# Kernel tuning notes

Hardware: AMD Instinct MI355X
Metric: run time of the kernel (lower is better)

The kernel has to match this reference:

```python
import jax, jax.numpy as jnp
import numpy as np
from jax import lax

L = 12        # transformer layers
H = 768       # d_model
NH = 12       # heads
HD = H // NH  # head dim
F = 2048      # ffn dim (torch TransformerEncoderLayer default)
V = 128       # vocab_size (level logits)
NLV = 128     # n_levels (rows of routed weight W)
B, S = 8, 512
EPS = 1e-5


def _layer_norm(x, g, b):
    mu = jnp.mean(x, axis=-1, keepdims=True)
    var = jnp.mean(jnp.square(x - mu), axis=-1, keepdims=True)
    return g * (x - mu) / jnp.sqrt(var + EPS) + b


def _encoder(x, layer_params):
    # torch nn.TransformerEncoderLayer, post-LN, ReLU, eval mode (no dropout)
    def block(h, p):
        Wqkv, bqkv, Wo, bo, g1, bb1, W1, b1f, W2, b2f, g2, bb2 = p
        qkv = h @ Wqkv.T + bqkv                      # [B,S,3H]
        q, k, v = jnp.split(qkv, 3, axis=-1)
        sh = (h.shape[0], h.shape[1], NH, HD)
        q, k, v = q.reshape(sh), k.reshape(sh), v.reshape(sh)
        scores = jnp.einsum('bqhd,bkhd->bhqk', q, k) / jnp.sqrt(jnp.asarray(HD, h.dtype))
        attn = jax.nn.softmax(scores, axis=-1)
        o = jnp.einsum('bhqk,bkhd->bqhd', attn, v).reshape(h.shape)
        o = o @ Wo.T + bo
        h = _layer_norm(h + o, g1, bb1)
        f = jnp.maximum(h @ W1.T + b1f, 0.0) @ W2.T + b2f
        h = _layer_norm(h + f, g2, bb2)
        return h, None
    x, _ = lax.scan(block, x, layer_params)
    return x


def setup_inputs() -> dict:
    key = jax.random.key(0)
    ks = jax.random.split(key, 20)
    s = 0.02
    rn = lambda k, shp: jax.random.normal(k, shp, jnp.float32) * s
    inp = {
        'level_ids': jax.random.randint(ks[0], (B, S), 0, V, jnp.int32),
        'sublevel_ids': jax.random.randint(ks[1], (B, S), 0, V, jnp.int32),
        'bin_emb': rn(ks[2], (V, H)),
        'sub_emb': rn(ks[3], (V, H)),
        'Wqkv': rn(ks[4], (L, 3 * H, H)),
        'bqkv': jnp.zeros((L, 3 * H), jnp.float32),
        'Wo': rn(ks[5], (L, H, H)),
        'bo': jnp.zeros((L, H), jnp.float32),
        'ln1_g': jnp.ones((L, H), jnp.float32),
        'ln1_b': jnp.zeros((L, H), jnp.float32),
        'W1': rn(ks[6], (L, F, H)),
        'b1': jnp.zeros((L, F), jnp.float32),
        'W2': rn(ks[7], (L, H, F)),
        'b2': jnp.zeros((L, H), jnp.float32),
        'ln2_g': jnp.ones((L, H), jnp.float32),
        'ln2_b': jnp.zeros((L, H), jnp.float32),
        'W_lm': rn(ks[8], (V, H)),
        'b_lm': jnp.zeros((V,), jnp.float32),
        'W': rn(ks[9], (NLV, H, V)),       # routed per-level weights
        'bias': jnp.zeros((NLV, V), jnp.float32),
    }
    return inp


def reference(level_ids, sublevel_ids, bin_emb, sub_emb, Wqkv, bqkv, Wo, bo,
              ln1_g, ln1_b, W1, b1, W2, b2, ln2_g, ln2_b, W_lm, b_lm, W, bias):
    # embedding: sum of two id tables (tabular bin/subbin embedding)
    x = bin_emb[level_ids] + sub_emb[sublevel_ids]            # [B,S,H]
    layer_params = (Wqkv, bqkv, Wo, bo, ln1_g, ln1_b, W1, b1, W2, b2, ln2_g, ln2_b)
    x = _encoder(x, layer_params)                              # [B,S,H]
    out = x @ W_lm.T + b_lm                                    # [B,S,V]
    ix = jnp.argmax(out, axis=-1)                              # [B,S] routing index
    # per-token weight gather + batched vec-mat: the irregular hot path
    Wg = W[ix]                                                 # [B,S,H,V]
    sublevel_out = jnp.einsum('bsh,bshv->bsv', x, Wg) + bias[ix]
    return (out, sublevel_out)
```

## Files before the change

### kernel.cpp

```cpp
#include <hip/hip_runtime.h>
#include <cstdint>
#include <cstddef>

#define TOK 4096
#define HD_ 64
#define NH_ 12
#define H_ 768
#define F_ 2048
#define V_ 128
#define L_ 12
#define SEQ 512
#define BQKV (3*H_)
#define BATCH 8

typedef _Float16 f16;
typedef _Float16 f16x8 __attribute__((ext_vector_type(8)));
typedef _Float16 f16x4 __attribute__((ext_vector_type(4)));
typedef float    f32x4 __attribute__((ext_vector_type(4)));

#define GLDS16(g, l) __builtin_amdgcn_global_load_lds( \
    (const __attribute__((address_space(1))) uint32_t*)(g), \
    (__attribute__((address_space(3))) uint32_t*)(l), 16, 0, 0)

__device__ __forceinline__ float wave_sum(float v) {
#pragma unroll
  for (int m = 32; m >= 1; m >>= 1) v += __shfl_xor(v, m);
  return v;
}

__device__ __forceinline__ void split16(float v, f16& h, f16& lo) {
  h = (f16)v;
  lo = (f16)((v - (float)h) * 2048.0f);
}

__device__ __forceinline__ int swz(int r, int c) {
  int byte = (r << 7) + (c << 1);
  byte ^= (r & 7) << 4;
  return byte >> 1;
}

__global__ __launch_bounds__(256)
void k_convert(const float* __restrict__ src, f16* __restrict__ h, f16* __restrict__ l,
               int n4, float scale) {
  int i = blockIdx.x * 256 + threadIdx.x;
  int stride = gridDim.x * 256;
  for (; i < n4; i += stride) {
    float4 v = ((const float4*)src)[i];
    v.x *= scale; v.y *= scale; v.z *= scale; v.w *= scale;
    f16x4 vh, vl;
    f16 a, b;
    split16(v.x, a, b); vh[0] = a; vl[0] = b;
    split16(v.y, a, b); vh[1] = a; vl[1] = b;
    split16(v.z, a, b); vh[2] = a; vl[2] = b;
    split16(v.w, a, b); vh[3] = a; vl[3] = b;
    ((f16x4*)h)[i] = vh;
    ((f16x4*)l)[i] = vl;
  }
}

__global__ __launch_bounds__(256)
void k_embed2(const int* __restrict__ lid, const int* __restrict__ sid,
              const float* __restrict__ be, const float* __restrict__ se,
              float* __restrict__ x, f16* __restrict__ xh, f16* __restrict__ xl) {
  int t = blockIdx.x;
  int li = lid[t], si = sid[t];
  const float* bp = be + (size_t)li * H_;
  const float* sp = se + (size_t)si * H_;
  size_t base = (size_t)t * H_;
#pragma unroll
  for (int j = 0; j < 3; ++j) {
    int hh = threadIdx.x + 256 * j;
    float v = bp[hh] + sp[hh];
    x[base + hh] = v;
    f16 a, b; split16(v, a, b);
    xh[base + hh] = a; xl[base + hh] = b;
  }
}

template<int BM, int BN, int MODE>
__global__ __launch_bounds__(256)
void k_gemm3(const f16* __restrict__ Ah, const f16* __restrict__ Al,
             const f16* __restrict__ Bh, const f16* __restrict__ Bl,
             const float* __restrict__ bias, float* __restrict__ C,
             f16* __restrict__ Ch, f16* __restrict__ Cl,
             int N, int K) {
  constexpr int MI = BM / 32, NJ = BN / 32;
  constexpr int IA = BM / 64, IB = BN / 64;
  constexpr int ABYT = BM * 64, BBYT = BN * 64;
  constexpr int BUFB = 2 * ABYT + 2 * BBYT;
  __shared__ __align__(16) char sm[2 * BUFB];
  const int tid = threadIdx.x;
  const int lane = tid & 63, wid = tid >> 6;
  const int wr = wid >> 1, wc = wid & 1;
  const int bm = blockIdx.x * BM, bn = blockIdx.y * BN;
  const size_t rs = (size_t)K * 2;

  const int srow = tid >> 2, schk = tid & 3;
  const char* ga[2][IA];
  const char* gb[2][IB];
#pragma unroll
  for (int u = 0; u < IA; ++u) {
    int row = u * 64 + srow;
    int c = schk ^ ((row >> 1) & 3);
    ga[0][u] = (const char*)Ah + (size_t)(bm + row) * rs + c * 16;
    ga[1][u] = (const char*)Al + (size_t)(bm + row) * rs + c * 16;
  }
#pragma unroll
  for (int u = 0; u < IB; ++u) {
    int row = u * 64 + srow;
    int c = schk ^ ((row >> 1) & 3);
    gb[0][u] = (const char*)Bh + (size_t)(bn + row) * rs + c * 16;
    gb[1][u] = (const char*)Bl + (size_t)(bn + row) * rs + c * 16;
  }

  const int rr = lane & 15, cgrp = lane >> 4;
  int aoff[MI][2], boff[NJ][2];
#pragma unroll
  for (int i = 0; i < MI; ++i) {
    int row = wr * (BM / 2) + i * 16 + rr;
    int sw = (cgrp ^ ((row >> 1) & 3)) * 16;
    aoff[i][0] = row * 64 + sw;
    aoff[i][1] = ABYT + row * 64 + sw;
  }
#pragma unroll
  for (int j = 0; j < NJ; ++j) {
    int row = wc * (BN / 2) + j * 16 + rr;
    int sw = (cgrp ^ ((row >> 1) & 3)) * 16;
    boff[j][0] = 2 * ABYT + row * 64 + sw;
    boff[j][1] = 2 * ABYT + BBYT + row * 64 + sw;
  }

  f32x4 aH[MI][NJ], aM[MI][NJ];
#pragma unroll
  for (int i = 0; i < MI; ++i)
#pragma unroll
    for (int j = 0; j < NJ; ++j)
#pragma unroll
      for (int q = 0; q < 4; ++q) { aH[i][j][q] = 0.0f; aM[i][j][q] = 0.0f; }

  auto STG = [&](int b) __attribute__((always_inline)) {
    char* base = sm + b * BUFB + wid * 1024;
#pragma unroll
    for (int u = 0; u < IA; ++u) {
      GLDS16(ga[0][u], base + u * 4096);
      GLDS16(ga[1][u], base + ABYT + u * 4096);
      ga[0][u] += 64; ga[1][u] += 64;
    }
#pragma unroll
    for (int u = 0; u < IB; ++u) {
      GLDS16(gb[0][u], base + 2 * ABYT + u * 4096);
      GLDS16(gb[1][u], base + 2 * ABYT + BBYT + u * 4096);
      gb[0][u] += 64; gb[1][u] += 64;
    }
  };

  auto CMP = [&](int b) __attribute__((always_inline)) {
    const char* base = sm + b * BUFB;
    f16x8 fbh[NJ], fbl[NJ];
#pragma unroll
    for (int j = 0; j < NJ; ++j) {
      fbh[j] = *(const f16x8*)(base + boff[j][0]);
      fbl[j] = *(const f16x8*)(base + boff[j][1]);
    }
#pragma unroll
    for (int i = 0; i < MI; ++i) {
      f16x8 fah = *(const f16x8*)(base + aoff[i][0]);
      f16x8 fal = *(const f16x8*)(base + aoff[i][1]);
#pragma unroll
      for (int j = 0; j < NJ; ++j) {
        aH[i][j] = __builtin_amdgcn_mfma_f32_16x16x32_f16(fah, fbh[j], aH[i][j], 0, 0, 0);
        aM[i][j] = __builtin_amdgcn_mfma_f32_16x16x32_f16(fah, fbl[j], aM[i][j], 0, 0, 0);
        aM[i][j] = __builtin_amdgcn_mfma_f32_16x16x32_f16(fal, fbh[j], aM[i][j], 0, 0, 0);
      }
    }
  };

  STG(0);
  __syncthreads();
  const int nst = K / 32;
  for (int s = 1; s < nst; s += 2) {
    STG(1); CMP(0);
    __syncthreads();
    if (s + 1 < nst) {
      STG(0); CMP(1);
      __syncthreads();
    }
  }
  CMP((nst - 1) & 1);

  const int r4 = (lane >> 4) * 4, cc = lane & 15;
#pragma unroll
  for (int i = 0; i < MI; ++i) {
#pragma unroll
    for (int j = 0; j < NJ; ++j) {
      int col = bn + wc * (BN / 2) + j * 16 + cc;
      float bz = bias[col];
#pragma unroll
      for (int q = 0; q < 4; ++q) {
        int row = bm + wr * (BM / 2) + i * 16 + r4 + q;
        float v = (aH[i][j][q] + aM[i][j][q] * (1.0f / 2048.0f)) * (1.0f / 64.0f) + bz;
        if (MODE == 0) {
          C[(size_t)row * N + col] = v;
        } else {
          if (MODE == 1) v = fmaxf(v, 0.0f);
          f16 a, b; split16(v, a, b);
          Ch[(size_t)row * N + col] = a;
          Cl[(size_t)row * N + col] = b;
        }
      }
    }
  }
}

__global__ __launch_bounds__(256)
void k_flash_mfma(const f16* __restrict__ ph, const f16* __restrict__ pl,
                  f16* __restrict__ oh, f16* __restrict__ ol) {
  __shared__ __align__(16) f16 VtH[4096];
  __shared__ __align__(16) f16 VtL[4096];
  __shared__ __align__(16) f16 PH[4096];
  __shared__ __align__(16) f16 PL[4096];
  __shared__ float PS[2][64];
  const int tid = threadIdx.x;
  const int lane = tid & 63, wid = tid >> 6;
  const int wr = wid >> 1, wc = wid & 1;
  const int qt = blockIdx.x, bh = blockIdx.y;
  const int b = bh / NH_, hd = bh % NH_;
  const int rr = lane & 15, kg = (lane >> 4) * 8;
  const size_t tok0 = (size_t)b * SEQ;

  f16x8 qfh[2][2], qfl[2][2];
#pragma unroll
  for (int ifr = 0; ifr < 2; ++ifr)
#pragma unroll
    for (int ks = 0; ks < 2; ++ks) {
      size_t g = (tok0 + qt * 64 + wr * 32 + ifr * 16 + rr) * (size_t)BQKV + hd * HD_ + ks * 32 + kg;
      qfh[ifr][ks] = *(const f16x8*)&ph[g];
      qfl[ifr][ks] = *(const f16x8*)&pl[g];
    }

  f32x4 oha[2][2], oma[2][2];
  f32x4 ps[2];
#pragma unroll
  for (int i = 0; i < 2; ++i) {
#pragma unroll
    for (int q = 0; q < 4; ++q) ps[i][q] = 0.0f;
#pragma unroll
    for (int j = 0; j < 2; ++j)
#pragma unroll
      for (int q = 0; q < 4; ++q) { oha[i][j][q] = 0.0f; oma[i][j][q] = 0.0f; }
  }

  const int vj = tid >> 2;
  const int vs = tid & 3;

  for (int kt = 0; kt < SEQ / 64; ++kt) {
    __syncthreads();
#pragma unroll
    for (int s = 0; s < 2; ++s) {
      int d0 = (vs + s * 4) * 8;
      size_t g = (tok0 + kt * 64 + vj) * (size_t)BQKV + 2 * H_ + hd * HD_ + d0;
      f16x8 vh8 = *(const f16x8*)&ph[g];
      f16x8 vl8 = *(const f16x8*)&pl[g];
#pragma unroll
      for (int u = 0; u < 8; ++u) {
        VtH[swz(d0 + u, vj)] = vh8[u];
        VtL[swz(d0 + u, vj)] = vl8[u];
      }
    }
    __syncthreads();
    f16x8 kfh[2][2], kfl[2][2];
#pragma unroll
    for (int jf = 0; jf < 2; ++jf)
#pragma unroll
      for (int ks = 0; ks < 2; ++ks) {
        size_t g = (tok0 + kt * 64 + wc * 32 + jf * 16 + rr) * (size_t)BQKV + H_ + hd * HD_ + ks * 32 + kg;
        kfh[jf][ks] = *(const f16x8*)&ph[g];
        kfl[jf][ks] = *(const f16x8*)&pl[g];
      }
    f32x4 sh[2][2], sm2[2][2];
#pragma unroll
    for (int i = 0; i < 2; ++i)
#pragma unroll
      for (int j = 0; j < 2; ++j)
#pragma unroll
        for (int q = 0; q < 4; ++q) { sh[i][j][q] = 0.0f; sm2[i][j][q] = 0.0f; }
#pragma unroll
    for (int ifr = 0; ifr < 2; ++ifr)
#pragma unroll
      for (int jf = 0; jf < 2; ++jf)
#pragma unroll
        for (int ks = 0; ks < 2; ++ks) {
          sh[ifr][jf] = __builtin_amdgcn_mfma_f32_16x16x32_f16(qfh[ifr][ks], kfh[jf][ks], sh[ifr][jf], 0, 0, 0);
          sm2[ifr][jf] = __builtin_amdgcn_mfma_f32_16x16x32_f16(qfh[ifr][ks], kfl[jf][ks], sm2[ifr][jf], 0, 0, 0);
          sm2[ifr][jf] = __builtin_amdgcn_mfma_f32_16x16x32_f16(qfl[ifr][ks], kfh[jf][ks], sm2[ifr][jf], 0, 0, 0);
        }
#pragma unroll
    for (int ifr = 0; ifr < 2; ++ifr)
#pragma unroll
      for (int jf = 0; jf < 2; ++jf) {
        int pj = wc * 32 + jf * 16 + rr;
#pragma unroll
        for (int q = 0; q < 4; ++q) {
          int pi = wr * 32 + ifr * 16 + (lane >> 4) * 4 + q;
          float sval = (sh[ifr][jf][q] + sm2[ifr][jf][q] * (1.0f / 2048.0f)) * 0.125f;
          float p = expf(sval);
          ps[ifr][q] += p;
          f16 a, b2; split16(p, a, b2);
          PH[swz(pi, pj)] = a;
          PL[swz(pi, pj)] = b2;
        }
      }
    __syncthreads();
#pragma unroll
    for (int ks = 0; ks < 2; ++ks) {
      f16x8 pfh[2], pfl[2], vfh[2], vfl[2];
#pragma unroll
      for (int ifr = 0; ifr < 2; ++ifr) {
        pfh[ifr] = *(const f16x8*)&PH[swz(wr * 32 + ifr * 16 + rr, ks * 32 + kg)];
        pfl[ifr] = *(const f16x8*)&PL[swz(wr * 32 + ifr * 16 + rr, ks * 32 + kg)];
      }
#pragma unroll
      for (int jf = 0; jf < 2; ++jf) {
        vfh[jf] = *(const f16x8*)&VtH[swz(wc * 32 + jf * 16 + rr, ks * 32 + kg)];
        vfl[jf] = *(const f16x8*)&VtL[swz(wc * 32 + jf * 16 + rr, ks * 32 + kg)];
      }
#pragma unroll
      for (int ifr = 0; ifr < 2; ++ifr)
#pragma unroll
        for (int jf = 0; jf < 2; ++jf) {
          oha[ifr][jf] = __builtin_amdgcn_mfma_f32_16x16x32_f16(pfh[ifr], vfh[jf], oha[ifr][jf], 0, 0, 0);
          oma[ifr][jf] = __builtin_amdgcn_mfma_f32_16x16x32_f16(pfh[ifr], vfl[jf], oma[ifr][jf], 0, 0, 0);
          oma[ifr][jf] = __builtin_amdgcn_mfma_f32_16x16x32_f16(pfl[ifr], vfh[jf], oma[ifr][jf], 0, 0, 0);
        }
    }
  }

#pragma unroll
  for (int ifr = 0; ifr < 2; ++ifr)
#pragma unroll
    for (int m = 1; m < 16; m <<= 1)
#pragma unroll
      for (int q = 0; q < 4; ++q) ps[ifr][q] += __shfl_xor(ps[ifr][q], m);
  if (rr == 0) {
#pragma unroll
    for (int ifr = 0; ifr < 2; ++ifr)
#pragma unroll
      for (int q = 0; q < 4; ++q)
        PS[wc][wr * 32 + ifr * 16 + (lane >> 4) * 4 + q] = ps[ifr][q];
  }
  __syncthreads();

#pragma unroll
  for (int ifr = 0; ifr < 2; ++ifr)
#pragma unroll
    for (int jf = 0; jf < 2; ++jf)
#pragma unroll
      for (int q = 0; q < 4; ++q) {
        int i = wr * 32 + ifr * 16 + (lane >> 4) * 4 + q;
        float inv = 1.0f / (PS[0][i] + PS[1][i]);
        float o = (oha[ifr][jf][q] + oma[ifr][jf][q] * (1.0f / 2048.0f)) * inv;
        size_t g = (tok0 + qt * 64 + i) * (size_t)H_ + hd * HD_ + wc * 32 + jf * 16 + rr;
        f16 a, b2; split16(o, a, b2);
        oh[g] = a; ol[g] = b2;
      }
}

__global__ __launch_bounds__(256)
void k_ln_res2(const float* __restrict__ xin, const float* __restrict__ y,
               const float* __restrict__ g, const float* __restrict__ bb,
               float* __restrict__ xout, f16* __restrict__ xh, f16* __restrict__ xl) {
  __shared__ float red[8];
  int t = blockIdx.x;
  const float* xr = xin + (size_t)t * H_;
  const float* yr = y + (size_t)t * H_;
  float v[3];
#pragma unroll
  for (int j = 0; j < 3; ++j) {
    int hh = threadIdx.x + 256 * j;
    v[j] = xr[hh] + yr[hh];
  }
  float s = v[0] + v[1] + v[2];
  s = wave_sum(s);
  int w = threadIdx.x >> 6;
  if ((threadIdx.x & 63) == 0) red[w] = s;
  __syncthreads();
  float mu = (red[0] + red[1] + red[2] + red[3]) * (1.0f / 768.0f);
  float q = 0.f;
#pragma unroll
  for (int j = 0; j < 3; ++j) { float d = v[j] - mu; q = fmaf(d, d, q); }
  q = wave_sum(q);
  if ((threadIdx.x & 63) == 0) red[4 + w] = q;
  __syncthreads();
  float var = (red[4] + red[5] + red[6] + red[7]) * (1.0f / 768.0f);
  float rinv = 1.0f / sqrtf(var + 1e-5f);
#pragma unroll
  for (int j = 0; j < 3; ++j) {
    int hh = threadIdx.x + 256 * j;
    float val = fmaf(g[hh], (v[j] - mu) * rinv, bb[hh]);
    size_t idx = (size_t)t * H_ + hh;
    xout[idx] = val;
    f16 a, b; split16(val, a, b);
    xh[idx] = a; xl[idx] = b;
  }
}

__global__ __launch_bounds__(64)
void k_argmax(const float* __restrict__ logits, int* __restrict__ ix) {
  int t = blockIdx.x, l = threadIdx.x;
  float v0 = logits[(size_t)t * V_ + l];
  float v1 = logits[(size_t)t * V_ + 64 + l];
  float best = v0; int bi = l;
  if (v1 > best) { best = v1; bi = 64 + l; }
#pragma unroll
  for (int m = 1; m < 64; m <<= 1) {
    float ov = __shfl_xor(best, m);
    int oi = __shfl_xor(bi, m);
    if (ov > best || (ov == best && oi < bi)) { best = ov; bi = oi; }
  }
  if (l == 0) ix[t] = bi;
}

__global__ __launch_bounds__(128)
void k_sublevel(const float* __restrict__ x, const float* __restrict__ W,
                const float* __restrict__ bias, const int* __restrict__ ix,
                float* __restrict__ out) {
  int t = blockIdx.x, v = threadIdx.x;
  int r = ix[t];
  const float* Wr = W + (size_t)r * H_ * V_;
  const float* xr = x + (size_t)t * H_;
  float acc = bias[(size_t)r * V_ + v];
#pragma unroll 8
  for (int h = 0; h < H_; ++h)
    acc = fmaf(xr[h], Wr[(size_t)h * V_ + v], acc);
  out[(size_t)t * V_ + v] = acc;
}

extern "C" void kernel_launch(void* const* d_in, const int* in_sizes, int n_in,
                              void* d_out, int out_size, void* d_ws, size_t ws_size,
                              hipStream_t stream) {
  const int*   lid  = (const int*)d_in[0];
  const int*   sid  = (const int*)d_in[1];
  const float* be   = (const float*)d_in[2];
  const float* se   = (const float*)d_in[3];
  const float* Wqkv = (const float*)d_in[4];
  const float* bqkv = (const float*)d_in[5];
  const float* Wo   = (const float*)d_in[6];
  const float* bo   = (const float*)d_in[7];
  const float* g1   = (const float*)d_in[8];
  const float* b1n  = (const float*)d_in[9];
  const float* W1   = (const float*)d_in[10];
  const float* b1f  = (const float*)d_in[11];
  const float* W2   = (const float*)d_in[12];
  const float* b2f  = (const float*)d_in[13];
  const float* g2   = (const float*)d_in[14];
  const float* b2n  = (const float*)d_in[15];
  const float* Wlm  = (const float*)d_in[16];
  const float* blm  = (const float*)d_in[17];
  const float* Wrt  = (const float*)d_in[18];
  const float* brt  = (const float*)d_in[19];

  char* ws = (char*)d_ws;
  float* x    = (float*)(ws + 0);
  f16*   xh   = (f16*)  (ws + 12582912);
  f16*   xl   = (f16*)  (ws + 18874368);
  f16*   qh   = (f16*)  (ws + 25165824);
  f16*   ql   = (f16*)  (ws + 44040192);
  f16*   midh = qh;
  f16*   midl = ql;
  f16*   ath  = (f16*)  (ws + 62914560);
  f16*   atl  = (f16*)  (ws + 69206016);
  float* bufY = (float*)(ws + 75497472);
  f16*   wsh  = (f16*)  (ws + 88080384);
  f16*   wsl  = (f16*)  (ws + 91619328);
  f16*   wlmh = (f16*)  (ws + 95158272);
  f16*   wlml = (f16*)  (ws + 95354880);
  int*   ix   = (int*)  (ws + 95551488);
  const size_t need = 95567872;
  if (ws_size < need) return;

  bool big = ws_size >= need + 265000000ull;
  f16 *bWqh = nullptr, *bWql = nullptr, *bWoh = nullptr, *bWol = nullptr,
      *bW1h = nullptr, *bW1l = nullptr, *bW2h = nullptr, *bW2l = nullptr;
  if (big) {
    char* p = ws + 95600640;
    bWqh = (f16*)p; p += 42467328;
    bWql = (f16*)p; p += 42467328;
    bWoh = (f16*)p; p += 14155776;
    bWol = (f16*)p; p += 14155776;
    bW1h = (f16*)p; p += 37748736;
    bW1l = (f16*)p; p += 37748736;
    bW2h = (f16*)p; p += 37748736;
    bW2l = (f16*)p; p += 37748736;
    k_convert<<<2048, 256, 0, stream>>>(Wqkv, bWqh, bWql, L_ * BQKV * H_ / 4, 64.f);
    k_convert<<<2048, 256, 0, stream>>>(Wo,   bWoh, bWol, L_ * H_ * H_ / 4, 64.f);
    k_convert<<<2048, 256, 0, stream>>>(W1,   bW1h, bW1l, L_ * F_ * H_ / 4, 64.f);
    k_convert<<<2048, 256, 0, stream>>>(W2,   bW2h, bW2l, L_ * H_ * F_ / 4, 64.f);
  }
  k_convert<<<96, 256, 0, stream>>>(Wlm, wlmh, wlml, V_ * H_ / 4, 64.f);

  float* out0 = (float*)d_out;
  float* out1 = out0 + (size_t)TOK * V_;

  k_embed2<<<TOK, 256, 0, stream>>>(lid, sid, be, se, x, xh, xl);

  for (int l = 0; l < L_; ++l) {
    const float* bqkv_l = bqkv + (size_t)l * BQKV;
    const float* bo_l   = bo   + (size_t)l * H_;
    const float* g1_l   = g1   + (size_t)l * H_;
    const float* b1n_l  = b1n  + (size_t)l * H_;
    const float* b1f_l  = b1f  + (size_t)l * F_;
    const float* b2f_l  = b2f  + (size_t)l * H_;
    const float* g2_l   = g2   + (size_t)l * H_;
    const float* b2n_l  = b2n  + (size_t)l * H_;

    const f16 *wh, *wl2;
    if (big) { wh = bWqh + (size_t)l * BQKV * H_; wl2 = bWql + (size_t)l * BQKV * H_; }
    else {
      k_convert<<<1728, 256, 0, stream>>>(Wqkv + (size_t)l * BQKV * H_, wsh, wsl, BQKV * H_ / 4, 64.f);
      wh = wsh; wl2 = wsl;
    }
    k_gemm3<64, 128, 2><<<dim3(TOK / 64, BQKV / 128), 256, 0, stream>>>(
        xh, xl, wh, wl2, bqkv_l, nullptr, qh, ql, BQKV, H_);
    k_flash_mfma<<<dim3(SEQ / 64, BATCH * NH_), 256, 0, stream>>>(qh, ql, ath, atl);
    if (big) { wh = bWoh + (size_t)l * H_ * H_; wl2 = bWol + (size_t)l * H_ * H_; }
    else {
      k_convert<<<576, 256, 0, stream>>>(Wo + (size_t)l * H_ * H_, wsh, wsl, H_ * H_ / 4, 64.f);
      wh = wsh; wl2 = wsl;
    }
    k_gemm3<64, 64, 0><<<dim3(TOK / 64, H_ / 64), 256, 0, stream>>>(
        ath, atl, wh, wl2, bo_l, bufY, nullptr, nullptr, H_, H_);
    k_ln_res2<<<TOK, 256, 0, stream>>>(x, bufY, g1_l, b1n_l, x, xh, xl);
    if (big) { wh = bW1h + (size_t)l * F_ * H_; wl2 = bW1l + (size_t)l * F_ * H_; }
    else {
      k_convert<<<1536, 256, 0, stream>>>(W1 + (size_t)l * F_ * H_, wsh, wsl, F_ * H_ / 4, 64.f);
      wh = wsh; wl2 = wsl;
    }
    k_gemm3<64, 128, 1><<<dim3(TOK / 64, F_ / 128), 256, 0, stream>>>(
        xh, xl, wh, wl2, b1f_l, nullptr, midh, midl, F_, H_);
    if (big) { wh = bW2h + (size_t)l * H_ * F_; wl2 = bW2l + (size_t)l * H_ * F_; }
    else {
      k_convert<<<1536, 256, 0, stream>>>(W2 + (size_t)l * H_ * F_, wsh, wsl, H_ * F_ / 4, 64.f);
      wh = wsh; wl2 = wsl;
    }
    k_gemm3<64, 64, 0><<<dim3(TOK / 64, H_ / 64), 256, 0, stream>>>(
        midh, midl, wh, wl2, b2f_l, bufY, nullptr, nullptr, H_, F_);
    k_ln_res2<<<TOK, 256, 0, stream>>>(x, bufY, g2_l, b2n_l, x, xh, xl);
  }

  k_gemm3<64, 64, 0><<<dim3(TOK / 64, V_ / 64), 256, 0, stream>>>(
      xh, xl, wlmh, wlml, blm, out0, nullptr, nullptr, V_, H_);
  k_argmax<<<TOK, 64, 0, stream>>>(out0, ix);
  k_sublevel<<<TOK, V_, 0, stream>>>(x, Wrt, brt, ix, out1);
}
```

Measured before the change: 3.779 ms.

## Triple-buffer GEMM staging and group routed sublevel matmul by level

Result: faster. 3.696 ms (-2.2%).

```diff
diff --git a/kernel.cpp b/kernel.cpp
--- a/kernel.cpp
+++ b/kernel.cpp
@@ -61,8 +61,10 @@
 __global__ __launch_bounds__(256)
 void k_embed2(const int* __restrict__ lid, const int* __restrict__ sid,
               const float* __restrict__ be, const float* __restrict__ se,
-              float* __restrict__ x, f16* __restrict__ xh, f16* __restrict__ xl) {
+              float* __restrict__ x, f16* __restrict__ xh, f16* __restrict__ xl,
+              int* __restrict__ counts) {
   int t = blockIdx.x;
+  if (t == 0 && threadIdx.x < V_) counts[threadIdx.x] = 0;
   int li = lid[t], si = sid[t];
   const float* bp = be + (size_t)li * H_;
   const float* sp = se + (size_t)si * H_;
@@ -79,7 +81,7 @@
 
 template<int BM, int BN, int MODE>
 __global__ __launch_bounds__(256)
-void k_gemm3(const f16* __restrict__ Ah, const f16* __restrict__ Al,
+void k_gemm4(const f16* __restrict__ Ah, const f16* __restrict__ Al,
              const f16* __restrict__ Bh, const f16* __restrict__ Bl,
              const float* __restrict__ bias, float* __restrict__ C,
              f16* __restrict__ Ch, f16* __restrict__ Cl,
@@ -88,7 +90,8 @@
   constexpr int IA = BM / 64, IB = BN / 64;
   constexpr int ABYT = BM * 64, BBYT = BN * 64;
   constexpr int BUFB = 2 * ABYT + 2 * BBYT;
-  __shared__ __align__(16) char sm[2 * BUFB];
+  constexpr int NGL = 2 * (IA + IB);
+  __shared__ __align__(16) char sm_[3 * BUFB];
   const int tid = threadIdx.x;
   const int lane = tid & 63, wid = tid >> 6;
   const int wr = wid >> 1, wc = wid & 1;
@@ -138,8 +141,8 @@
 #pragma unroll
       for (int q = 0; q < 4; ++q) { aH[i][j][q] = 0.0f; aM[i][j][q] = 0.0f; }
 
-  auto STG = [&](int b) __attribute__((always_inline)) {
-    char* base = sm + b * BUFB + wid * 1024;
+  auto STG = [&](char* bufbase) __attribute__((always_inline)) {
+    char* base = bufbase + wid * 1024;
 #pragma unroll
     for (int u = 0; u < IA; ++u) {
       GLDS16(ga[0][u], base + u * 4096);
@@ -154,8 +157,7 @@
     }
   };
 
-  auto CMP = [&](int b) __attribute__((always_inline)) {
-    const char* base = sm + b * BUFB;
+  auto CMP = [&](const char* base) __attribute__((always_inline)) {
     f16x8 fbh[NJ], fbl[NJ];
 #pragma unroll
     for (int j = 0; j < NJ; ++j) {
@@ -175,18 +177,23 @@
     }
   };
 
-  STG(0);
-  __syncthreads();
+  char* b0 = sm_;
+  char* b1 = sm_ + BUFB;
+  char* b2 = sm_ + 2 * BUFB;
+  STG(b0);
   const int nst = K / 32;
-  for (int s = 1; s < nst; s += 2) {
-    STG(1); CMP(0);
-    __syncthreads();
+  for (int s = 0; s < nst; ++s) {
     if (s + 1 < nst) {
-      STG(0); CMP(1);
-      __syncthreads();
-    }
-  }
-  CMP((nst - 1) & 1);
+      STG(b1);
+      asm volatile("s_waitcnt vmcnt(%0)" :: "i"(NGL) : "memory");
+    } else {
+      asm volatile("s_waitcnt vmcnt(0)" ::: "memory");
+    }
+    __builtin_amdgcn_s_barrier();
+    __builtin_amdgcn_sched_barrier(0);
+    CMP(b0);
+    char* tmp = b0; b0 = b1; b1 = b2; b2 = tmp;
+  }
 
   const int r4 = (lane >> 4) * 4, cc = lane & 15;
 #pragma unroll
@@ -405,7 +412,8 @@
 }
 
 __global__ __launch_bounds__(64)
-void k_argmax(const float* __restrict__ logits, int* __restrict__ ix) {
+void k_argmax(const float* __restrict__ logits, int* __restrict__ ix,
+              int* __restrict__ counts) {
   int t = blockIdx.x, l = threadIdx.x;
   float v0 = logits[(size_t)t * V_ + l];
   float v1 = logits[(size_t)t * V_ + 64 + l];
@@ -417,22 +425,102 @@
     int oi = __shfl_xor(bi, m);
     if (ov > best || (ov == best && oi < bi)) { best = ov; bi = oi; }
   }
-  if (l == 0) ix[t] = bi;
+  if (l == 0) { ix[t] = bi; atomicAdd(&counts[bi], 1); }
 }
 
 __global__ __launch_bounds__(128)
-void k_sublevel(const float* __restrict__ x, const float* __restrict__ W,
-                const float* __restrict__ bias, const int* __restrict__ ix,
-                float* __restrict__ out) {
-  int t = blockIdx.x, v = threadIdx.x;
+void k_prep(const int* __restrict__ counts, int* __restrict__ offsets,
+            int* __restrict__ cursors, int4* __restrict__ chunks,
+            int* __restrict__ nchunks) {
+  __shared__ int s[128];
+  int r = threadIdx.x;
+  int c = counts[r];
+  s[r] = c; __syncthreads();
+  for (int d = 1; d < 128; d <<= 1) {
+    int v = (r >= d) ? s[r - d] : 0; __syncthreads();
+    s[r] += v; __syncthreads();
+  }
+  int off = s[r] - c;
+  offsets[r] = off;
+  cursors[r] = 0;
+  int nch = (c + 15) >> 4;
+  __syncthreads();
+  s[r] = nch; __syncthreads();
+  for (int d = 1; d < 128; d <<= 1) {
+    int v = (r >= d) ? s[r - d] : 0; __syncthreads();
+    s[r] += v; __syncthreads();
+  }
+  int cb = s[r] - nch;
+  for (int u = 0; u < nch; ++u) {
+    int rem = c - u * 16;
+    chunks[cb + u] = make_int4(r, off + u * 16, rem < 16 ? rem : 16, 0);
+  }
+  if (r == 127) *nchunks = s[127];
+}
+
+__global__ __launch_bounds__(256)
+void k_scatter(const int* __restrict__ ix, const int* __restrict__ offsets,
+               int* __restrict__ cursors, int* __restrict__ bucket) {
+  int t = blockIdx.x * 256 + threadIdx.x;
   int r = ix[t];
-  const float* Wr = W + (size_t)r * H_ * V_;
-  const float* xr = x + (size_t)t * H_;
-  float acc = bias[(size_t)r * V_ + v];
-#pragma unroll 8
-  for (int h = 0; h < H_; ++h)
-    acc = fmaf(xr[h], Wr[(size_t)h * V_ + v], acc);
-  out[(size_t)t * V_ + v] = acc;
+  int p = atomicAdd(&cursors[r], 1);
+  bucket[offsets[r] + p] = t;
+}
+
+__global__ __launch_bounds__(256)
+void k_sublevel2(const float* __restrict__ x, const float* __restrict__ W,
+                 const float* __restrict__ bias, const int* __restrict__ bucket,
+                 const int4* __restrict__ chunks, const int* __restrict__ nchunks,
+                 float* __restrict__ out) {
+  int c = blockIdx.x;
+  if (c >= *nchunks) return;
+  int4 ch = chunks[c];
+  int r = ch.x, ts = ch.y, nt = ch.z;
+  __shared__ int toks[16];
+  __shared__ float accs[16][V_];
+  int tid = threadIdx.x;
+  if (tid < 16) toks[tid] = bucket[ts + (tid < nt ? tid : 0)];
+  __syncthreads();
+  const int lane = tid & 63;
+  const int wv = tid >> 6;
+  const int vh = wv & 1, kh = wv >> 1;
+  const int v = vh * 64 + lane;
+  const float* Wr = W + (size_t)r * (H_ * V_);
+  int tk[16];
+#pragma unroll
+  for (int t = 0; t < 16; ++t) tk[t] = toks[t];
+  float acc[16];
+#pragma unroll
+  for (int t = 0; t < 16; ++t) acc[t] = 0.f;
+
+  for (int k0 = kh * 384; k0 < kh * 384 + 384; k0 += 64) {
+    float xv[16];
+#pragma unroll
+    for (int t = 0; t < 16; ++t)
+      xv[t] = x[(size_t)tk[t] * H_ + k0 + lane];
+#pragma unroll 4
+    for (int kk = 0; kk < 64; ++kk) {
+      float w = Wr[(size_t)(k0 + kk) * V_ + v];
+#pragma unroll
+      for (int t = 0; t < 16; ++t) {
+        float xs = __uint_as_float(
+            __builtin_amdgcn_readlane(__float_as_uint(xv[t]), kk));
+        acc[t] = fmaf(xs, w, acc[t]);
+      }
+    }
+  }
+  if (kh == 1) {
+#pragma unroll
+    for (int t = 0; t < 16; ++t) accs[t][v] = acc[t];
+  }
+  __syncthreads();
+  if (kh == 0) {
+    float bz = bias[(size_t)r * V_ + v];
+#pragma unroll
+    for (int t = 0; t < 16; ++t) {
+      if (t < nt) out[(size_t)tk[t] * V_ + v] = acc[t] + accs[t][v] + bz;
+    }
+  }
 }
 
 extern "C" void kernel_launch(void* const* d_in, const int* in_sizes, int n_in,
@@ -475,10 +563,16 @@
   f16*   wlmh = (f16*)  (ws + 95158272);
   f16*   wlml = (f16*)  (ws + 95354880);
   int*   ix   = (int*)  (ws + 95551488);
-  const size_t need = 95567872;
+  int*   counts  = (int*)(ws + 95567872);
+  int*   cursors = (int*)(ws + 95568384);
+  int*   offsets = (int*)(ws + 95568896);
+  int4*  chunks  = (int4*)(ws + 95569920);
+  int*   nchunks = (int*)(ws + 95576064);
+  int*   bucket  = (int*)(ws + 95576320);
+  const size_t need = 95592704;
   if (ws_size < need) return;
 
-  bool big = ws_size >= need + 265000000ull;
+  bool big = ws_size >= 95600640ull + 265000000ull;
   f16 *bWqh = nullptr, *bWql = nullptr, *bWoh = nullptr, *bWol = nullptr,
       *bW1h = nullptr, *bW1l = nullptr, *bW2h = nullptr, *bW2l = nullptr;
   if (big) {
@@ -501,7 +595,7 @@
   float* out0 = (float*)d_out;
   float* out1 = out0 + (size_t)TOK * V_;
 
-  k_embed2<<<TOK, 256, 0, stream>>>(lid, sid, be, se, x, xh, xl);
+  k_embed2<<<TOK, 256, 0, stream>>>(lid, sid, be, se, x, xh, xl, counts);
 
   for (int l = 0; l < L_; ++l) {
     const float* bqkv_l = bqkv + (size_t)l * BQKV;
@@ -519,7 +613,7 @@
       k_convert<<<1728, 256, 0, stream>>>(Wqkv + (size_t)l * BQKV * H_, wsh, wsl, BQKV * H_ / 4, 64.f);
       wh = wsh; wl2 = wsl;
     }
-    k_gemm3<64, 128, 2><<<dim3(TOK / 64, BQKV / 128), 256, 0, stream>>>(
+    k_gemm4<64, 128, 2><<<dim3(TOK / 64, BQKV / 128), 256, 0, stream>>>(
         xh, xl, wh, wl2, bqkv_l, nullptr, qh, ql, BQKV, H_);
     k_flash_mfma<<<dim3(SEQ / 64, BATCH * NH_), 256, 0, stream>>>(qh, ql, ath, atl);
     if (big) { wh = bWoh + (size_t)l * H_ * H_; wl2 = bWol + (size_t)l * H_ * H_; }
@@ -527,7 +621,7 @@
       k_convert<<<576, 256, 0, stream>>>(Wo + (size_t)l * H_ * H_, wsh, wsl, H_ * H_ / 4, 64.f);
       wh = wsh; wl2 = wsl;
     }
-    k_gemm3<64, 64, 0><<<dim3(TOK / 64, H_ / 64), 256, 0, stream>>>(
+    k_gemm4<64, 64, 0><<<dim3(TOK / 64, H_ / 64), 256, 0, stream>>>(
         ath, atl, wh, wl2, bo_l, bufY, nullptr, nullptr, H_, H_);
     k_ln_res2<<<TOK, 256, 0, stream>>>(x, bufY, g1_l, b1n_l, x, xh, xl);
     if (big) { wh = bW1h + (size_t)l * F_ * H_; wl2 = bW1l + (size_t)l * F_ * H_; }
@@ -535,20 +629,22 @@
       k_convert<<<1536, 256, 0, stream>>>(W1 + (size_t)l * F_ * H_, wsh, wsl, F_ * H_ / 4, 64.f);
       wh = wsh; wl2 = wsl;
     }
-    k_gemm3<64, 128, 1><<<dim3(TOK / 64, F_ / 128), 256, 0, stream>>>(
+    k_gemm4<64, 128, 1><<<dim3(TOK / 64, F_ / 128), 256, 0, stream>>>(
         xh, xl, wh, wl2, b1f_l, nullptr, midh, midl, F_, H_);
     if (big) { wh = bW2h + (size_t)l * H_ * F_; wl2 = bW2l + (size_t)l * H_ * F_; }
     else {
       k_convert<<<1536, 256, 0, stream>>>(W2 + (size_t)l * H_ * F_, wsh, wsl, H_ * F_ / 4, 64.f);
       wh = wsh; wl2 = wsl;
     }
-    k_gemm3<64, 64, 0><<<dim3(TOK / 64, H_ / 64), 256, 0, stream>>>(
+    k_gemm4<64, 64, 0><<<dim3(TOK / 64, H_ / 64), 256, 0, stream>>>(
         midh, midl, wh, wl2, b2f_l, bufY, nullptr, nullptr, H_, F_);
     k_ln_res2<<<TOK, 256, 0, stream>>>(x, bufY, g2_l, b2n_l, x, xh, xl);
   }
 
-  k_gemm3<64, 64, 0><<<dim3(TOK / 64, V_ / 64), 256, 0, stream>>>(
+  k_gemm4<64, 64, 0><<<dim3(TOK / 64, V_ / 64), 256, 0, stream>>>(
       xh, xl, wlmh, wlml, blm, out0, nullptr, nullptr, V_, H_);
-  k_argmax<<<TOK, 64, 0, stream>>>(out0, ix);
-  k_sublevel<<<TOK, V_, 0, stream>>>(x, Wrt, brt, ix, out1);
-}
+  k_argmax<<<TOK, 64, 0, stream>>>(out0, ix, counts);
+  k_prep<<<1, 128, 0, stream>>>(counts, offsets, cursors, chunks, nchunks);
+  k_scatter<<<TOK / 256, 256, 0, stream>>>(ix, offsets, cursors, bucket);
+  k_sublevel2<<<384, 256, 0, stream>>>(x, Wrt, brt, bucket, chunks, nchunks, out1);
+}
```
